# Performance work log

Measured on AMD Instinct MI355X. Metric: run time of the kernel, lower is better.

## Reference

```python
import jax, jax.numpy as jnp
import numpy as np

# Tier config (cumulative d_model [256,1024,2048], cumulative heads [4,12,24], d_k=64)
TIER_OWN = [256, 768, 1024]      # per-tier own hidden dims
HEAD_OUT = [256, 512, 768]       # n_heads_per_tier[i] * d_k
NHS = [4, 8, 12]
DKS = [64, 64, 64]
RANK = 8
IN_OFF = np.cumsum([0] + TIER_OWN)    # [0,256,1024,2048]
OUT_OFF = np.cumsum([0] + HEAD_OUT)   # [0,256,768,1536]


def _block_ut_weight(key, in_dims, out_dims):
    """Full (sum_in, sum_out) matrix with lower-triangular blocks zeroed."""
    io = np.cumsum([0] + list(in_dims))
    oo = np.cumsum([0] + list(out_dims))
    n = len(in_dims)
    mask = np.zeros((io[-1], oo[-1]), dtype=np.float32)
    for i in range(n):
        for j in range(i, n):
            mask[io[i]:io[i + 1], oo[j]:oo[j + 1]] = 1.0
    W = jax.random.normal(key, (io[-1], oo[-1]), dtype=jnp.float32) * 0.02
    return W * jnp.asarray(mask)


def setup_inputs() -> dict:
    key = jax.random.key(0)
    ks = jax.random.split(key, 16)
    B, T, D = 4, 1024, 2048
    x = jax.random.normal(ks[0], (B, T, D), dtype=jnp.float32)
    W_Q = _block_ut_weight(ks[1], TIER_OWN, HEAD_OUT)
    W_K = _block_ut_weight(ks[2], TIER_OWN, HEAD_OUT)
    W_V = _block_ut_weight(ks[3], TIER_OWN, HEAD_OUT)
    W_O = _block_ut_weight(ks[4], HEAD_OUT, TIER_OWN)
    # feedback for tiers 0 and 1 (tier 2 has no higher tiers)
    hi0 = TIER_OWN[1] + TIER_OWN[2]  # 1792
    hi1 = TIER_OWN[2]                # 1024
    FK0 = jax.random.normal(ks[5], (hi0, NHS[0] * RANK), dtype=jnp.float32) * 0.02
    PK0 = jax.random.normal(ks[6], (NHS[0], RANK, DKS[0]), dtype=jnp.float32) * 0.01
    FV0 = jax.random.normal(ks[7], (hi0, NHS[0] * RANK), dtype=jnp.float32) * 0.02
    PV0 = jax.random.normal(ks[8], (NHS[0], RANK, DKS[0]), dtype=jnp.float32) * 0.01
    FK1 = jax.random.normal(ks[9], (hi1, NHS[1] * RANK), dtype=jnp.float32) * 0.02
    PK1 = jax.random.normal(ks[10], (NHS[1], RANK, DKS[1]), dtype=jnp.float32) * 0.01
    FV1 = jax.random.normal(ks[11], (hi1, NHS[1] * RANK), dtype=jnp.float32) * 0.02
    PV1 = jax.random.normal(ks[12], (NHS[1], RANK, DKS[1]), dtype=jnp.float32) * 0.01
    return dict(x=x, W_Q=W_Q, W_K=W_K, W_V=W_V, W_O=W_O,
                FK0=FK0, PK0=PK0, FV0=FV0, PV0=PV0,
                FK1=FK1, PK1=PK1, FV1=FV1, PV1=PV1)


def _forward(x, W_Q, W_K, W_V, W_O, FK0, PK0, FV0, PV0, FK1, PK1, FV1, PV1):
    B, T, _ = x.shape
    Q_all = x @ W_Q
    K_all = x @ W_K
    V_all = x @ W_V
    causal = jnp.tril(jnp.ones((T, T), dtype=bool))
    fb = {0: (FK0, PK0, FV0, PV0), 1: (FK1, PK1, FV1, PV1)}
    head_outs = []
    for tier in range(3):
        nh, dk = NHS[tier], DKS[tier]
        dim = nh * dk
        o = int(OUT_OFF[tier])
        Q = Q_all[..., o:o + dim]
        K = K_all[..., o:o + dim]
        V = V_all[..., o:o + dim]
        if tier in fb:
            Fk, Pk, Fv, Pv = fb[tier]
            h_hi = x[..., int(IN_OFF[tier + 1]):]  # higher tiers' hidden
            c_k = (h_hi @ Fk).reshape(B, T, nh, RANK)
            K = K + jnp.einsum('bthr,hrd->bthd', c_k, Pk).reshape(B, T, dim)
            c_v = (h_hi @ Fv).reshape(B, T, nh, RANK)
            V = V + jnp.einsum('bthr,hrd->bthd', c_v, Pv).reshape(B, T, dim)
        Qh = Q.reshape(B, T, nh, dk).transpose(0, 2, 1, 3)
        Kh = K.reshape(B, T, nh, dk).transpose(0, 2, 1, 3)
        Vh = V.reshape(B, T, nh, dk).transpose(0, 2, 1, 3)
        scores = jnp.einsum('bhqd,bhkd->bhqk', Qh, Kh) / jnp.sqrt(jnp.float32(dk))
        scores = jnp.where(causal, scores, jnp.float32(-1e30))
        attn = jax.nn.softmax(scores, axis=-1)
        out = jnp.einsum('bhqk,bhkd->bhqd', attn, Vh)
        head_outs.append(out.transpose(0, 2, 1, 3).reshape(B, T, dim))
    return jnp.concatenate(head_outs, axis=-1) @ W_O


def reference(x, W_Q, W_K, W_V, W_O, FK0, PK0, FV0, PV0, FK1, PK1, FV1, PV1):
    return _forward(x, W_Q, W_K, W_V, W_O, FK0, PK0, FV0, PV0, FK1, PK1, FV1, PV1)
```

## Files before the change

kernel.cpp:

```cpp
#include <hip/hip_runtime.h>


typedef short bf16x8 __attribute__((ext_vector_type(8)));
typedef float floatx4 __attribute__((ext_vector_type(4)));

__device__ __forceinline__ unsigned short f2bf(float f) {
  unsigned u = __builtin_bit_cast(unsigned, f);
  u += 0x7fffu + ((u >> 16) & 1u);
  return (unsigned short)(u >> 16);
}

__device__ __forceinline__ void gload_lds16(const unsigned short* g, unsigned short* l) {
  __builtin_amdgcn_global_load_lds((const __attribute__((address_space(1))) unsigned int*)g,
                                   (__attribute__((address_space(3))) unsigned int*)l, 16, 0, 0);
}

__global__ __launch_bounds__(256) void k_prep(
    const float* __restrict__ x, unsigned short* __restrict__ X16,
    const float* __restrict__ WQ, const float* __restrict__ WK, const float* __restrict__ WV,
    const float* __restrict__ FK0, const float* __restrict__ PK0,
    const float* __restrict__ FV0, const float* __restrict__ PV0,
    const float* __restrict__ FK1, const float* __restrict__ PK1,
    const float* __restrict__ FV1, const float* __restrict__ PV1,
    unsigned short* __restrict__ WTQKV,
    const float* __restrict__ WO, unsigned short* __restrict__ WTO) {
  __shared__ float tile[32][33];
  __shared__ float Fs[32][9];
  __shared__ float Ps[8][32];
  const int bid = blockIdx.x;
  const int tid = threadIdx.x;
  if (bid < 8192) {
    int i = bid * 256 + tid;
    float4 v = ((const float4*)x)[i];
    union { unsigned short u[4]; uint2 v2; } o;
    o.u[0] = f2bf(v.x); o.u[1] = f2bf(v.y); o.u[2] = f2bf(v.z); o.u[3] = f2bf(v.w);
    ((uint2*)X16)[i] = o.v2;
    return;
  }
  const int tx = tid & 31, ty = tid >> 5;
  if (bid < 17408) {
    int t = bid - 8192;
    int k0 = (t & 63) * 32, n0 = (t >> 6) * 32;
    const float* src; int nboff;
    if (n0 < 1536)      { src = WQ; nboff = n0; }
    else if (n0 < 3072) { src = WK; nboff = n0 - 1536; }
    else                { src = WV; nboff = n0 - 3072; }
#pragma unroll
    for (int j = 0; j < 4; ++j) {
      int kk = ty + j * 8;
      tile[kk][tx] = src[(size_t)(k0 + kk) * 1536 + nboff + tx];
    }
    int corrsel = 0; const float* Fsrc = nullptr; const float* Psrc = nullptr;
    int h = 0, d0 = 0, fs = 0, koff = 0;
    if (n0 >= 1536) {
      bool isK = (n0 < 3072);
      int np0 = isK ? (n0 - 1536) : (n0 - 3072);
      if (np0 < 256) {
        if (k0 >= 256) { corrsel = 1; Fsrc = isK ? FK0 : FV0; Psrc = isK ? PK0 : PV0;
                         h = np0 >> 6; d0 = np0 & 63; fs = 32; koff = k0 - 256; }
      } else if (np0 < 768) {
        if (k0 >= 1024) { corrsel = 1; Fsrc = isK ? FK1 : FV1; Psrc = isK ? PK1 : PV1;
                          h = (np0 - 256) >> 6; d0 = (np0 - 256) & 63; fs = 64; koff = k0 - 1024; }
      }
    }
    if (corrsel) {
      Fs[tid >> 3][tid & 7] = Fsrc[(size_t)(koff + (tid >> 3)) * fs + h * 8 + (tid & 7)];
      Ps[tid >> 5][tid & 31] = Psrc[h * 512 + (tid >> 5) * 64 + d0 + (tid & 31)];
    }
    __syncthreads();
#pragma unroll
    for (int j = 0; j < 4; ++j) {
      int nn = ty + j * 8;
      float v = tile[tx][nn];
      if (corrsel) {
        float c = 0.f;
#pragma unroll
        for (int r = 0; r < 8; ++r) c += Fs[tx][r] * Ps[r][nn];
        v += c;
      }
      WTQKV[(size_t)(n0 + nn) * 2048 + k0 + tx] = f2bf(v);
    }
  } else {
    int t = bid - 17408;
    int k0 = (t % 48) * 32, n0 = (t / 48) * 32;
#pragma unroll
    for (int j = 0; j < 4; ++j)
      tile[ty + j * 8][tx] = WO[(size_t)(k0 + ty + j * 8) * 2048 + n0 + tx];
    __syncthreads();
#pragma unroll
    for (int j = 0; j < 4; ++j)
      WTO[(size_t)(n0 + ty + j * 8) * 1536 + k0 + tx] = f2bf(tile[tx][ty + j * 8]);
  }
}

template <bool OUT_BF16, int MODE>
__global__ __launch_bounds__(256) void k_gemm_bt(const unsigned short* __restrict__ A,
                                                 const unsigned short* __restrict__ Bt,
                                                 void* __restrict__ C, int M, int N, int K) {
  __shared__ unsigned short As[128 * 64];
  __shared__ unsigned short Bs[128 * 64];
  const int tid = threadIdx.x;
  const int wave = tid >> 6, lane = tid & 63;
  const int qd = lane >> 4, ln = lane & 15;
  const int bm = blockIdx.y * 128, bn = blockIdx.x * 128;
  const int wr = wave >> 1, wc = wave & 1;
  int Keff;
  if (MODE == 0) Keff = (bn < 256) ? 256 : (bn < 768 ? 1024 : 2048);
  else           Keff = (bn < 256) ? 256 : (bn < 1024 ? 768 : 1536);
  floatx4 acc[4][4];
#pragma unroll
  for (int i = 0; i < 4; ++i)
#pragma unroll
    for (int j = 0; j < 4; ++j) acc[i][j] = (floatx4){0.f, 0.f, 0.f, 0.f};
  const int rl = lane >> 3;
  const int sg = (lane & 7) ^ rl;
  const unsigned short* gA = A + (size_t)(bm + wave * 32 + rl) * K + sg * 8;
  const unsigned short* gB = Bt + (size_t)(bn + wave * 32 + rl) * K + sg * 8;
  unsigned short* lA = As + wave * 2048;
  unsigned short* lB = Bs + wave * 2048;
  const int l7 = ln & 7;
  for (int k0 = 0; k0 < Keff; k0 += 64) {
    __syncthreads();
#pragma unroll
    for (int i = 0; i < 4; ++i) {
      gload_lds16(gA + (size_t)8 * i * K + k0, lA + i * 512);
      gload_lds16(gB + (size_t)8 * i * K + k0, lB + i * 512);
    }
    __syncthreads();
#pragma unroll
    for (int h = 0; h < 2; ++h) {
      bf16x8 af[4], bfr[4];
#pragma unroll
      for (int mi = 0; mi < 4; ++mi)
        af[mi] = *(const bf16x8*)(As + (wr * 64 + mi * 16 + ln) * 64 + ((h * 4 + qd) ^ l7) * 8);
#pragma unroll
      for (int ni = 0; ni < 4; ++ni)
        bfr[ni] = *(const bf16x8*)(Bs + (wc * 64 + ni * 16 + ln) * 64 + ((h * 4 + qd) ^ l7) * 8);
#pragma unroll
      for (int mi = 0; mi < 4; ++mi)
#pragma unroll
        for (int ni = 0; ni < 4; ++ni)
          acc[mi][ni] = __builtin_amdgcn_mfma_f32_16x16x32_bf16(af[mi], bfr[ni], acc[mi][ni], 0, 0, 0);
    }
  }
#pragma unroll
  for (int mi = 0; mi < 4; ++mi)
#pragma unroll
    for (int r = 0; r < 4; ++r) {
      int row = bm + wr * 64 + mi * 16 + qd * 4 + r;
#pragma unroll
      for (int ni = 0; ni < 4; ++ni) {
        int col = bn + wc * 64 + ni * 16 + ln;
        if (OUT_BF16)
          ((unsigned short*)C)[(size_t)row * N + col] = f2bf(acc[mi][ni][r]);
        else
          ((float*)C)[(size_t)row * N + col] = acc[mi][ni][r];
      }
    }
}

__global__ void k_transpose_v(const unsigned short* __restrict__ QKV,
                              unsigned short* __restrict__ VT) {
  __shared__ unsigned short t[64 * 65];
  const int tt = blockIdx.x * 64, dt = blockIdx.y * 64, b = blockIdx.z;
  const int tid = threadIdx.x;
  const int r = tid >> 3, c0 = (tid & 7) * 8;
#pragma unroll
  for (int i = 0; i < 2; ++i) {
    int tok = r + i * 32;
    union { uint4 v; unsigned short u[8]; } vv;
    vv.v = *(const uint4*)(QKV + (size_t)(b * 1024 + tt + tok) * 4608 + 3072 + dt + c0);
#pragma unroll
    for (int j = 0; j < 8; ++j) t[tok * 65 + c0 + j] = vv.u[j];
  }
  __syncthreads();
#pragma unroll
  for (int i = 0; i < 2; ++i) {
    int d = r + i * 32;
    union { uint4 v; unsigned short u[8]; } vv;
#pragma unroll
    for (int j = 0; j < 8; ++j) vv.u[j] = t[(c0 + j) * 65 + d];
    *(uint4*)(VT + ((size_t)b * 1536 + dt + d) * 1024 + tt + c0) = vv.v;
  }
}

#define LDP 72
__global__ __launch_bounds__(256) void k_attn(const unsigned short* __restrict__ QKV,
                                              const unsigned short* __restrict__ VT,
                                              unsigned short* __restrict__ Oout) {
  __shared__ unsigned short Ks[64 * 64];
  __shared__ unsigned short VTs[64 * 64];
  __shared__ unsigned short Pl[4][2][16 * LDP];
  const int tid = threadIdx.x;
  const int wave = tid >> 6, lane = tid & 63;
  const int qd = lane >> 4, ln = lane & 15;
  const int qb = (int)gridDim.x - 1 - (int)blockIdx.x;
  const int gh = blockIdx.y, b = blockIdx.z;
  const int T = 1024, LD = 4608;
  const size_t rowbase = (size_t)b * T * LD;
  const int qcol = 64 * gh, kcol = 1536 + 64 * gh;
  const unsigned short* VTg = VT + ((size_t)b * 1536 + 64 * gh) * 1024;
  const float SCALE = 0.18033688f;
  const int q0 = qb * 128 + wave * 16;

  bf16x8 aq[2][2];
#pragma unroll
  for (int j = 0; j < 2; ++j) {
    const unsigned short* qp = QKV + rowbase + (size_t)(q0 + j * 64 + ln) * LD + qcol;
    aq[j][0] = *(const bf16x8*)(qp + qd * 8);
    aq[j][1] = *(const bf16x8*)(qp + 32 + qd * 8);
  }
  floatx4 Oacc[2][4];
#pragma unroll
  for (int j = 0; j < 2; ++j)
#pragma unroll
    for (int i = 0; i < 4; ++i) Oacc[j][i] = (floatx4){0.f, 0.f, 0.f, 0.f};
  float l_lane[2] = {0.f, 0.f};

  const int drow = lane >> 3;
  const int dgrp = (lane & 7) ^ drow;
  const unsigned short* gK = QKV + rowbase + (size_t)(wave * 16 + drow) * LD + kcol + dgrp * 8;
  const unsigned short* gV = VTg + (size_t)(wave * 16 + drow) * 1024 + dgrp * 8;
  unsigned short* lK = Ks + wave * 16 * 64;
  unsigned short* lV = VTs + wave * 16 * 64;
  const int l7 = ln & 7;

  const int ntiles = 2 * qb + 2;
  for (int jt = 0; jt < ntiles; ++jt) {
    const int jk = jt * 64;
    __syncthreads();
    gload_lds16(gK + (size_t)jk * LD, lK);
    gload_lds16(gK + (size_t)(jk + 8) * LD, lK + 512);
    gload_lds16(gV + jk, lV);
    gload_lds16(gV + 8 * 1024 + jk, lV + 512);
    __syncthreads();

#pragma unroll
    for (int j = 0; j < 2; ++j) {
      if (j == 0 && jt == ntiles - 1) continue;
      floatx4 Sc[4];
#pragma unroll
      for (int h = 0; h < 4; ++h) {
        Sc[h] = (floatx4){0.f, 0.f, 0.f, 0.f};
        bf16x8 a0 = *(const bf16x8*)(Ks + (h * 16 + ln) * 64 + (qd ^ l7) * 8);
        bf16x8 a1 = *(const bf16x8*)(Ks + (h * 16 + ln) * 64 + ((4 + qd) ^ l7) * 8);
        Sc[h] = __builtin_amdgcn_mfma_f32_16x16x32_bf16(a0, aq[j][0], Sc[h], 0, 0, 0);
        Sc[h] = __builtin_amdgcn_mfma_f32_16x16x32_bf16(a1, aq[j][1], Sc[h], 0, 0, 0);
      }
      const bool diag = (jt == 2 * qb + j);
      const int qrow = q0 + j * 64 + ln;
      unsigned short* pw = Pl[wave][j];
#pragma unroll
      for (int h = 0; h < 4; ++h) {
        union { unsigned short u[4]; uint2 v; } pk;
#pragma unroll
        for (int r = 0; r < 4; ++r) {
          float v = fminf(Sc[h][r] * SCALE, 80.f);
          float p = __builtin_amdgcn_exp2f(v);
          if (diag) {
            int key = jk + h * 16 + qd * 4 + r;
            if (key > qrow) p = 0.f;
          }
          l_lane[j] += p;
          pk.u[r] = f2bf(p);
        }
        *(uint2*)(pw + ln * LDP + h * 16 + qd * 4) = pk.v;
      }
      __asm__ volatile("s_waitcnt lgkmcnt(0)" ::: "memory");
      bf16x8 pa0 = *(const bf16x8*)(pw + ln * LDP + qd * 8);
      bf16x8 pa1 = *(const bf16x8*)(pw + ln * LDP + 32 + qd * 8);
#pragma unroll
      for (int nc = 0; nc < 4; ++nc) {
        bf16x8 bv0 = *(const bf16x8*)(VTs + (nc * 16 + ln) * 64 + (qd ^ l7) * 8);
        bf16x8 bv1 = *(const bf16x8*)(VTs + (nc * 16 + ln) * 64 + ((4 + qd) ^ l7) * 8);
        Oacc[j][nc] = __builtin_amdgcn_mfma_f32_16x16x32_bf16(pa0, bv0, Oacc[j][nc], 0, 0, 0);
        Oacc[j][nc] = __builtin_amdgcn_mfma_f32_16x16x32_bf16(pa1, bv1, Oacc[j][nc], 0, 0, 0);
      }
    }
  }
#pragma unroll
  for (int j = 0; j < 2; ++j) {
    float l = l_lane[j];
    l += __shfl_xor(l, 16, 64);
    l += __shfl_xor(l, 32, 64);
#pragma unroll
    for (int r = 0; r < 4; ++r) {
      float inv = 1.0f / __shfl(l, qd * 4 + r, 64);
      size_t row = (size_t)b * T + q0 + j * 64 + qd * 4 + r;
#pragma unroll
      for (int nc = 0; nc < 4; ++nc)
        Oout[row * 1536 + 64 * gh + nc * 16 + ln] = f2bf(Oacc[j][nc][r] * inv);
    }
  }
}

extern "C" void kernel_launch(void* const* d_in, const int* in_sizes, int n_in,
                              void* d_out, int out_size, void* d_ws, size_t ws_size,
                              hipStream_t stream) {
  (void)in_sizes; (void)n_in; (void)out_size; (void)ws_size;
  const float* x   = (const float*)d_in[0];
  const float* WQ  = (const float*)d_in[1];
  const float* WK  = (const float*)d_in[2];
  const float* WV  = (const float*)d_in[3];
  const float* WO  = (const float*)d_in[4];
  const float* FK0 = (const float*)d_in[5];
  const float* PK0 = (const float*)d_in[6];
  const float* FV0 = (const float*)d_in[7];
  const float* PV0 = (const float*)d_in[8];
  const float* FK1 = (const float*)d_in[9];
  const float* PK1 = (const float*)d_in[10];
  const float* FV1 = (const float*)d_in[11];
  const float* PV1 = (const float*)d_in[12];

  char* ws = (char*)d_ws;
  unsigned short* X16   = (unsigned short*)(ws + 0);
  unsigned short* VTb   = X16;
  unsigned short* WTQKV = (unsigned short*)(ws + 16777216);
  unsigned short* QKV   = (unsigned short*)(ws + 35651584);
  unsigned short* ATT   = (unsigned short*)(ws + 73400320);
  unsigned short* WTO   = (unsigned short*)(ws + 85983232);

  k_prep<<<20480, 256, 0, stream>>>(x, X16, WQ, WK, WV,
                                    FK0, PK0, FV0, PV0, FK1, PK1, FV1, PV1,
                                    WTQKV, WO, WTO);
  k_gemm_bt<true, 0><<<dim3(36, 32), 256, 0, stream>>>(X16, WTQKV, QKV, 4096, 4608, 2048);
  k_transpose_v<<<dim3(16, 24, 4), 256, 0, stream>>>(QKV, VTb);
  k_attn<<<dim3(8, 24, 4), 256, 0, stream>>>(QKV, VTb, ATT);
  k_gemm_bt<false, 1><<<dim3(16, 32), 256, 0, stream>>>(ATT, WTO, d_out, 4096, 2048, 1536);
}
```

Baseline: 334.3 us.

## Enlarge attention key tiles to 128 and schedule GEMM blocks heaviest-first

The attention kernel now loads 128-key K and V^T tiles per iteration instead of 64, with a new XOR swizzle for the wider V^T tile. This halves the number of barrier and load rounds per query block and widens the P·V MFMA chain. Separately, both GEMMs switch to a 1D grid that launches the column tiles with the largest effective K first, so the block-triangular work is balanced across the machine. In exchange, shared memory per block grows and the score array per wave doubles, which may raise register pressure.

Result: no change. 332.1 us (-0.7%).

```diff
diff --git a/kernel.cpp b/kernel.cpp
--- a/kernel.cpp
+++ b/kernel.cpp
@@ -102,7 +102,17 @@
   const int tid = threadIdx.x;
   const int wave = tid >> 6, lane = tid & 63;
   const int qd = lane >> 4, ln = lane & 15;
-  const int bm = blockIdx.y * 128, bn = blockIdx.x * 128;
+  int idx = blockIdx.x, bx, by;
+  if (MODE == 0) {
+    if (idx < 960)       { bx = 6 + idx % 30; by = idx / 30; }
+    else if (idx < 1088) { int t = idx - 960; bx = 2 + (t & 3); by = t >> 2; }
+    else                 { int t = idx - 1088; bx = t & 1; by = t >> 1; }
+  } else {
+    if (idx < 256)       { bx = 8 + (idx & 7); by = idx >> 3; }
+    else if (idx < 448)  { int t = idx - 256; bx = 2 + t % 6; by = t / 6; }
+    else                 { int t = idx - 448; bx = t & 1; by = t >> 1; }
+  }
+  const int bm = by * 128, bn = bx * 128;
   const int wr = wave >> 1, wc = wave & 1;
   int Keff;
   if (MODE == 0) Keff = (bn < 256) ? 256 : (bn < 768 ? 1024 : 2048);
@@ -184,13 +194,13 @@
   }
 }
 
-#define LDP 72
+#define LDP 136
 __global__ __launch_bounds__(256) void k_attn(const unsigned short* __restrict__ QKV,
                                               const unsigned short* __restrict__ VT,
                                               unsigned short* __restrict__ Oout) {
-  __shared__ unsigned short Ks[64 * 64];
-  __shared__ unsigned short VTs[64 * 64];
-  __shared__ unsigned short Pl[4][2][16 * LDP];
+  __shared__ unsigned short Ks[128 * 64];
+  __shared__ unsigned short VTs[64 * 128];
+  __shared__ unsigned short Pl[4][16 * LDP];
   const int tid = threadIdx.x;
   const int wave = tid >> 6, lane = tid & 63;
   const int qd = lane >> 4, ln = lane & 15;
@@ -217,47 +227,59 @@
     for (int i = 0; i < 4; ++i) Oacc[j][i] = (floatx4){0.f, 0.f, 0.f, 0.f};
   float l_lane[2] = {0.f, 0.f};
 
-  const int drow = lane >> 3;
-  const int dgrp = (lane & 7) ^ drow;
-  const unsigned short* gK = QKV + rowbase + (size_t)(wave * 16 + drow) * LD + kcol + dgrp * 8;
-  const unsigned short* gV = VTg + (size_t)(wave * 16 + drow) * 1024 + dgrp * 8;
-  unsigned short* lK = Ks + wave * 16 * 64;
-  unsigned short* lV = VTs + wave * 16 * 64;
+  const int rk = lane >> 3;
+  const int gk = ((lane & 7) ^ rk) * 8;
+  const unsigned short* gK = QKV + rowbase + (size_t)(wave * 32 + rk) * LD + kcol + gk;
+  unsigned short* lK = Ks + wave * 32 * 64;
+  const int rv = lane >> 4;
+  const int cv = lane & 15;
+  unsigned short* lV = VTs + wave * 16 * 128;
+  const unsigned short* gVrow[4];
+  int gvcol[4];
+#pragma unroll
+  for (int i = 0; i < 4; ++i) {
+    int d = wave * 16 + 4 * i + rv;
+    gVrow[i] = VTg + (size_t)d * 1024;
+    gvcol[i] = (cv ^ (4 * i + rv)) * 8;
+  }
   const int l7 = ln & 7;
 
-  const int ntiles = 2 * qb + 2;
-  for (int jt = 0; jt < ntiles; ++jt) {
-    const int jk = jt * 64;
-    __syncthreads();
-    gload_lds16(gK + (size_t)jk * LD, lK);
-    gload_lds16(gK + (size_t)(jk + 8) * LD, lK + 512);
-    gload_lds16(gV + jk, lV);
-    gload_lds16(gV + 8 * 1024 + jk, lV + 512);
+  for (int jt = 0; jt <= qb; ++jt) {
+    const int jk = jt * 128;
+    const bool diag = (jt == qb);
+    __syncthreads();
+#pragma unroll
+    for (int i = 0; i < 4; ++i) {
+      gload_lds16(gK + (size_t)(jk + 8 * i) * LD, lK + i * 512);
+      gload_lds16(gVrow[i] + jk + gvcol[i], lV + i * 512);
+    }
     __syncthreads();
 
 #pragma unroll
     for (int j = 0; j < 2; ++j) {
-      if (j == 0 && jt == ntiles - 1) continue;
-      floatx4 Sc[4];
-#pragma unroll
-      for (int h = 0; h < 4; ++h) {
+      const bool dj0 = diag && (j == 0);
+      const int hmax = dj0 ? 4 : 8;
+      floatx4 Sc[8];
+#pragma unroll
+      for (int h = 0; h < 8; ++h) {
+        if (h >= hmax) continue;
         Sc[h] = (floatx4){0.f, 0.f, 0.f, 0.f};
         bf16x8 a0 = *(const bf16x8*)(Ks + (h * 16 + ln) * 64 + (qd ^ l7) * 8);
         bf16x8 a1 = *(const bf16x8*)(Ks + (h * 16 + ln) * 64 + ((4 + qd) ^ l7) * 8);
         Sc[h] = __builtin_amdgcn_mfma_f32_16x16x32_bf16(a0, aq[j][0], Sc[h], 0, 0, 0);
         Sc[h] = __builtin_amdgcn_mfma_f32_16x16x32_bf16(a1, aq[j][1], Sc[h], 0, 0, 0);
       }
-      const bool diag = (jt == 2 * qb + j);
       const int qrow = q0 + j * 64 + ln;
-      unsigned short* pw = Pl[wave][j];
-#pragma unroll
-      for (int h = 0; h < 4; ++h) {
+      unsigned short* pw = Pl[wave];
+#pragma unroll
+      for (int h = 0; h < 8; ++h) {
+        if (h >= hmax) continue;
         union { unsigned short u[4]; uint2 v; } pk;
 #pragma unroll
         for (int r = 0; r < 4; ++r) {
           float v = fminf(Sc[h][r] * SCALE, 80.f);
           float p = __builtin_amdgcn_exp2f(v);
-          if (diag) {
+          if (diag && (j == 0 || h >= 4)) {
             int key = jk + h * 16 + qd * 4 + r;
             if (key > qrow) p = 0.f;
           }
@@ -267,14 +289,22 @@
         *(uint2*)(pw + ln * LDP + h * 16 + qd * 4) = pk.v;
       }
       __asm__ volatile("s_waitcnt lgkmcnt(0)" ::: "memory");
-      bf16x8 pa0 = *(const bf16x8*)(pw + ln * LDP + qd * 8);
-      bf16x8 pa1 = *(const bf16x8*)(pw + ln * LDP + 32 + qd * 8);
+      const int smax = dj0 ? 2 : 4;
+      bf16x8 pa[4];
+#pragma unroll
+      for (int s = 0; s < 4; ++s) {
+        if (s >= smax) continue;
+        pa[s] = *(const bf16x8*)(pw + ln * LDP + s * 32 + qd * 8);
+      }
 #pragma unroll
       for (int nc = 0; nc < 4; ++nc) {
-        bf16x8 bv0 = *(const bf16x8*)(VTs + (nc * 16 + ln) * 64 + (qd ^ l7) * 8);
-        bf16x8 bv1 = *(const bf16x8*)(VTs + (nc * 16 + ln) * 64 + ((4 + qd) ^ l7) * 8);
-        Oacc[j][nc] = __builtin_amdgcn_mfma_f32_16x16x32_bf16(pa0, bv0, Oacc[j][nc], 0, 0, 0);
-        Oacc[j][nc] = __builtin_amdgcn_mfma_f32_16x16x32_bf16(pa1, bv1, Oacc[j][nc], 0, 0, 0);
+        const int d = nc * 16 + ln;
+#pragma unroll
+        for (int s = 0; s < 4; ++s) {
+          if (s >= smax) continue;
+          bf16x8 bv = *(const bf16x8*)(VTs + d * 128 + (((s * 4 + qd) ^ ln) & 15) * 8);
+          Oacc[j][nc] = __builtin_amdgcn_mfma_f32_16x16x32_bf16(pa[s], bv, Oacc[j][nc], 0, 0, 0);
+        }
       }
     }
   }
@@ -323,8 +353,8 @@
   k_prep<<<20480, 256, 0, stream>>>(x, X16, WQ, WK, WV,
                                     FK0, PK0, FV0, PV0, FK1, PK1, FV1, PV1,
                                     WTQKV, WO, WTO);
-  k_gemm_bt<true, 0><<<dim3(36, 32), 256, 0, stream>>>(X16, WTQKV, QKV, 4096, 4608, 2048);
+  k_gemm_bt<true, 0><<<1152, 256, 0, stream>>>(X16, WTQKV, QKV, 4096, 4608, 2048);
   k_transpose_v<<<dim3(16, 24, 4), 256, 0, stream>>>(QKV, VTb);
   k_attn<<<dim3(8, 24, 4), 256, 0, stream>>>(QKV, VTb, ATT);
-  k_gemm_bt<false, 1><<<dim3(16, 32), 256, 0, stream>>>(ATT, WTO, d_out, 4096, 2048, 1536);
-}
+  k_gemm_bt<false, 1><<<512, 256, 0, stream>>>(ATT, WTO, d_out, 4096, 2048, 1536);
+}
```
